# Performance work log

Hardware: AMD Instinct MI355X
Metric: run time of the kernel (lower is better)

## Reference

```python
import jax, jax.numpy as jnp
import numpy as np


def _dct_mats(N):
    # torch_dct.dct with norm=None: X_k = 2 * sum_n x_n cos(pi*(2n+1)k/(2N))
    # torch_dct.idct with norm=None is its exact inverse:
    #   x_n = (1/N) * (X_0/2 + sum_{k>=1} X_k cos(pi*(2n+1)k/(2N)))
    n = np.arange(N)
    k = np.arange(N)
    ang = np.pi * (2 * n[None, :] + 1) * k[:, None] / (2 * N)  # [k, n]
    cosang = np.cos(ang)
    D = (2.0 * cosang).astype(np.float32)                      # [k, n] DCT-II matrix
    scale = np.where(k == 0, 0.5, 1.0) / N                     # k=0 halved, /N overall
    Dinv = (cosang.T * scale[None, :]).astype(np.float32)      # [n, k] inverse matrix
    return jnp.asarray(D), jnp.asarray(Dinv)


def setup_inputs() -> dict:
    key = jax.random.key(0)
    k1, k2 = jax.random.split(key)
    B, C, H, W = 16, 28, 256, 256
    x = jax.random.normal(k1, (B, C, H, W), dtype=jnp.float32)
    weight = jax.random.normal(k2, (H, W, C), dtype=jnp.float32) * 0.02
    return {"x": x, "weight": weight}


def reference(x, weight):
    B, C, H, W = x.shape
    D, Dinv = _dct_mats(C)
    xt = jnp.transpose(x, (0, 2, 3, 1))            # [B, H, W, C]
    xd = jnp.einsum('bhwn,kn->bhwk', xt, D)        # DCT-II along channel dim
    xd = xd * weight                               # per-pixel spectral filter
    out = jnp.einsum('bhwk,nk->bhwn', xd, Dinv)    # inverse DCT along channel dim
    return jnp.transpose(out, (0, 3, 1, 2))        # back to [B, C, H, W]
```

## Files before the change

kernel.cpp:

```cpp
#include <hip/hip_runtime.h>

#define C_DIM 28
#define HALF 14
#define HW 65536
#define ITER 2
#define THREADS 256
#define GRID 2048

namespace {

constexpr double K_PI = 3.14159265358979323846;

constexpr double cos_taylor(double u) {
    double u2 = u * u;
    double term = 1.0, sum = 1.0;
    for (int i = 1; i <= 12; ++i) {
        term *= -u2 / (double)((2 * i - 1) * (2 * i));
        sum += term;
    }
    return sum;
}

constexpr double cos_pi_over56(int t) {
    t %= 112;
    if (t < 0) t += 112;
    double sign = 1.0;
    if (t > 56) t = 112 - t;
    if (t > 28) { t = 56 - t; sign = -1.0; }
    return sign * cos_taylor(K_PI * (double)t / 56.0);
}

struct Tables {
    float D[C_DIM][HALF];
    float Dinv[HALF][C_DIM];
};

constexpr Tables make_tables() {
    Tables t{};
    for (int k = 0; k < C_DIM; ++k)
        for (int n = 0; n < HALF; ++n)
            t.D[k][n] = (float)(2.0 * cos_pi_over56((2 * n + 1) * k));
    for (int n = 0; n < HALF; ++n)
        for (int k = 0; k < C_DIM; ++k)
            t.Dinv[n][k] = (float)(cos_pi_over56((2 * n + 1) * k) *
                                   ((k == 0) ? 0.5 : 1.0) / (double)C_DIM);
    return t;
}

constexpr Tables TBL = make_tables();

}

__global__ __launch_bounds__(THREADS) void spedct_kernel(
    const float* __restrict__ x,
    const float* __restrict__ w,
    float* __restrict__ out) {

    const int t  = blockIdx.x * THREADS + threadIdx.x;
    const int hw = t & (HW - 1);
    const int b0 = t >> 16;

    float wv[C_DIM];
    const float4* wp4 = (const float4*)(w + (size_t)hw * C_DIM);
#pragma unroll
    for (int i = 0; i < 7; ++i) {
        float4 v = wp4[i];
        wv[4 * i + 0] = v.x; wv[4 * i + 1] = v.y;
        wv[4 * i + 2] = v.z; wv[4 * i + 3] = v.w;
    }

    const size_t bstride = (size_t)8 * C_DIM * HW;
    const float* xp = x   + (size_t)b0 * C_DIM * HW + hw;
    float*       op = out + (size_t)b0 * C_DIM * HW + hw;

    float xv[2][C_DIM];
#pragma unroll
    for (int n = 0; n < C_DIM; ++n)
        xv[0][n] = __builtin_nontemporal_load(xp + (size_t)n * HW);

#pragma unroll
    for (int i = 0; i < ITER; ++i) {
        if (i + 1 < ITER) {
            const float* xn = xp + (size_t)(i + 1) * bstride;
#pragma unroll
            for (int n = 0; n < C_DIM; ++n)
                xv[i + 1][n] = __builtin_nontemporal_load(xn + (size_t)n * HW);
        }
        const float* xc = xv[i];

        float s[HALF], u[HALF];
#pragma unroll
        for (int n = 0; n < HALF; ++n) {
            s[n] = xc[n] + xc[27 - n];
            u[n] = xc[n] - xc[27 - n];
        }

        float xd[C_DIM];
#pragma unroll
        for (int k = 0; k < C_DIM; ++k)
            xd[k] = TBL.D[k][0] * ((k & 1) ? u[0] : s[0]);
#pragma unroll
        for (int n = 1; n < HALF; ++n) {
#pragma unroll
            for (int k = 0; k < C_DIM; ++k)
                xd[k] = fmaf(TBL.D[k][n], (k & 1) ? u[n] : s[n], xd[k]);
        }

#pragma unroll
        for (int k = 0; k < C_DIM; ++k) xd[k] *= wv[k];

        float e[HALF], f[HALF];
#pragma unroll
        for (int n = 0; n < HALF; ++n) {
            e[n] = TBL.Dinv[n][0] * xd[0];
            f[n] = TBL.Dinv[n][1] * xd[1];
        }
#pragma unroll
        for (int j = 1; j < HALF; ++j) {
#pragma unroll
            for (int n = 0; n < HALF; ++n) {
                e[n] = fmaf(TBL.Dinv[n][2 * j],     xd[2 * j],     e[n]);
                f[n] = fmaf(TBL.Dinv[n][2 * j + 1], xd[2 * j + 1], f[n]);
            }
        }

        float* oo = op + (size_t)i * bstride;
#pragma unroll
        for (int n = 0; n < HALF; ++n) {
            __builtin_nontemporal_store(e[n] + f[n], &oo[(size_t)n * HW]);
            __builtin_nontemporal_store(e[n] - f[n], &oo[(size_t)(27 - n) * HW]);
        }
    }
}

extern "C" void kernel_launch(void* const* d_in, const int* in_sizes, int n_in,
                              void* d_out, int out_size, void* d_ws, size_t ws_size,
                              hipStream_t stream) {
    const float* x = (const float*)d_in[0];
    const float* w = (const float*)d_in[1];
    float* out = (float*)d_out;

    spedct_kernel<<<dim3(GRID), dim3(THREADS), 0, stream>>>(x, w, out);
}
```

Baseline: 204.9 us.

## Process two adjacent pixels per thread with float2 loads instead of two batches

Each thread now handles two neighbouring pixels of one batch image, using 8-byte vector loads and stores of x and out in place of a loop over two batch images per thread. The weight is loaded for both pixels and no longer reused across batches, and the paired float arithmetic may map to packed FMA instructions. The intent is wider memory transactions and packed math; the cost is losing weight reuse across batches (more weight traffic) and higher register pressure from holding two pixel vectors.

```diff
diff --git a/kernel.cpp b/kernel.cpp
--- a/kernel.cpp
+++ b/kernel.cpp
@@ -3,7 +3,6 @@
 #define C_DIM 28
 #define HALF 14
 #define HW 65536
-#define ITER 2
 #define THREADS 256
 #define GRID 2048
 
@@ -49,6 +48,9 @@
 
 constexpr Tables TBL = make_tables();
 
+typedef float f2v __attribute__((ext_vector_type(2)));
+typedef float f4v __attribute__((ext_vector_type(4)));
+
 }
 
 __global__ __launch_bounds__(THREADS) void spedct_kernel(
@@ -56,80 +58,93 @@
     const float* __restrict__ w,
     float* __restrict__ out) {
 
-    const int t  = blockIdx.x * THREADS + threadIdx.x;
-    const int hw = t & (HW - 1);
-    const int b0 = t >> 16;
+    const int t   = blockIdx.x * THREADS + threadIdx.x;
+    const int b   = t >> 15;
+    const int hw0 = (t & 32767) << 1;
 
-    float wv[C_DIM];
-    const float4* wp4 = (const float4*)(w + (size_t)hw * C_DIM);
+    const float* xp = x   + (size_t)b * C_DIM * HW + hw0;
+    float*       op = out + (size_t)b * C_DIM * HW + hw0;
+
+    f2v xv[C_DIM];
 #pragma unroll
-    for (int i = 0; i < 7; ++i) {
-        float4 v = wp4[i];
-        wv[4 * i + 0] = v.x; wv[4 * i + 1] = v.y;
-        wv[4 * i + 2] = v.z; wv[4 * i + 3] = v.w;
+    for (int n = 0; n < C_DIM; ++n)
+        xv[n] = __builtin_nontemporal_load((const f2v*)(xp + (size_t)n * HW));
+
+    f2v s[HALF], u[HALF];
+#pragma unroll
+    for (int n = 0; n < HALF; ++n) {
+        s[n].x = xv[n].x + xv[27 - n].x;
+        s[n].y = xv[n].y + xv[27 - n].y;
+        u[n].x = xv[n].x - xv[27 - n].x;
+        u[n].y = xv[n].y - xv[27 - n].y;
     }
 
-    const size_t bstride = (size_t)8 * C_DIM * HW;
-    const float* xp = x   + (size_t)b0 * C_DIM * HW + hw;
-    float*       op = out + (size_t)b0 * C_DIM * HW + hw;
+    const f4v* wp4 = (const f4v*)(w + (size_t)hw0 * C_DIM);
+    f4v w0[7], w1[7];
+#pragma unroll
+    for (int q = 0; q < 7; ++q) w0[q] = wp4[q];
+#pragma unroll
+    for (int q = 0; q < 7; ++q) w1[q] = wp4[7 + q];
 
-    float xv[2][C_DIM];
+    f2v xd[C_DIM];
 #pragma unroll
-    for (int n = 0; n < C_DIM; ++n)
-        xv[0][n] = __builtin_nontemporal_load(xp + (size_t)n * HW);
+    for (int k = 0; k < C_DIM; ++k) {
+        const float c = TBL.D[k][0];
+        xd[k].x = c * ((k & 1) ? u[0].x : s[0].x);
+        xd[k].y = c * ((k & 1) ? u[0].y : s[0].y);
+    }
+#pragma unroll
+    for (int n = 1; n < HALF; ++n) {
+#pragma unroll
+        for (int k = 0; k < C_DIM; ++k) {
+            const float c = TBL.D[k][n];
+            if (k & 1) {
+                xd[k].x = fmaf(c, u[n].x, xd[k].x);
+                xd[k].y = fmaf(c, u[n].y, xd[k].y);
+            } else {
+                xd[k].x = fmaf(c, s[n].x, xd[k].x);
+                xd[k].y = fmaf(c, s[n].y, xd[k].y);
+            }
+        }
+    }
 
 #pragma unroll
-    for (int i = 0; i < ITER; ++i) {
-        if (i + 1 < ITER) {
-            const float* xn = xp + (size_t)(i + 1) * bstride;
+    for (int q = 0; q < 7; ++q) {
 #pragma unroll
-            for (int n = 0; n < C_DIM; ++n)
-                xv[i + 1][n] = __builtin_nontemporal_load(xn + (size_t)n * HW);
+        for (int i = 0; i < 4; ++i) {
+            xd[4 * q + i].x *= w0[q][i];
+            xd[4 * q + i].y *= w1[q][i];
         }
-        const float* xc = xv[i];
+    }
 
-        float s[HALF], u[HALF];
+    f2v e[HALF], f[HALF];
+#pragma unroll
+    for (int n = 0; n < HALF; ++n) {
+        e[n].x = TBL.Dinv[n][0] * xd[0].x;
+        e[n].y = TBL.Dinv[n][0] * xd[0].y;
+        f[n].x = TBL.Dinv[n][1] * xd[1].x;
+        f[n].y = TBL.Dinv[n][1] * xd[1].y;
+    }
+#pragma unroll
+    for (int j = 1; j < HALF; ++j) {
 #pragma unroll
         for (int n = 0; n < HALF; ++n) {
-            s[n] = xc[n] + xc[27 - n];
-            u[n] = xc[n] - xc[27 - n];
+            const float ce = TBL.Dinv[n][2 * j];
+            const float cf = TBL.Dinv[n][2 * j + 1];
+            e[n].x = fmaf(ce, xd[2 * j].x, e[n].x);
+            e[n].y = fmaf(ce, xd[2 * j].y, e[n].y);
+            f[n].x = fmaf(cf, xd[2 * j + 1].x, f[n].x);
+            f[n].y = fmaf(cf, xd[2 * j + 1].y, f[n].y);
         }
-
-        float xd[C_DIM];
-#pragma unroll
-        for (int k = 0; k < C_DIM; ++k)
-            xd[k] = TBL.D[k][0] * ((k & 1) ? u[0] : s[0]);
-#pragma unroll
-        for (int n = 1; n < HALF; ++n) {
-#pragma unroll
-            for (int k = 0; k < C_DIM; ++k)
-                xd[k] = fmaf(TBL.D[k][n], (k & 1) ? u[n] : s[n], xd[k]);
-        }
+    }
 
 #pragma unroll
-        for (int k = 0; k < C_DIM; ++k) xd[k] *= wv[k];
-
-        float e[HALF], f[HALF];
-#pragma unroll
-        for (int n = 0; n < HALF; ++n) {
-            e[n] = TBL.Dinv[n][0] * xd[0];
-            f[n] = TBL.Dinv[n][1] * xd[1];
-        }
-#pragma unroll
-        for (int j = 1; j < HALF; ++j) {
-#pragma unroll
-            for (int n = 0; n < HALF; ++n) {
-                e[n] = fmaf(TBL.Dinv[n][2 * j],     xd[2 * j],     e[n]);
-                f[n] = fmaf(TBL.Dinv[n][2 * j + 1], xd[2 * j + 1], f[n]);
-            }
-        }
-
-        float* oo = op + (size_t)i * bstride;
-#pragma unroll
-        for (int n = 0; n < HALF; ++n) {
-            __builtin_nontemporal_store(e[n] + f[n], &oo[(size_t)n * HW]);
-            __builtin_nontemporal_store(e[n] - f[n], &oo[(size_t)(27 - n) * HW]);
-        }
+    for (int n = 0; n < HALF; ++n) {
+        f2v lo, hi;
+        lo.x = e[n].x + f[n].x;  lo.y = e[n].y + f[n].y;
+        hi.x = e[n].x - f[n].x;  hi.y = e[n].y - f[n].y;
+        __builtin_nontemporal_store(lo, (f2v*)(op + (size_t)n * HW));
+        __builtin_nontemporal_store(hi, (f2v*)(op + (size_t)(27 - n) * HW));
     }
 }
 
```

Measured after the change: 228.6 us. 11.6% more time.
